# Kernel tuning notes

Hardware: AMD Instinct MI355X
Metric: run time of the kernel (lower is better)

Reference implementation:

```python
import jax, jax.numpy as jnp
import numpy as np

B = 16          # graphs per batch
N = 8192        # nodes per graph (equal-size graphs)
D = 256         # in_channels
RATIO = 0.5
K = int(np.ceil(RATIO * N))   # nodes kept per graph (PyG: ceil(ratio*N))
E = 2_097_152   # total edges (~avg_degree 16)


def setup_inputs() -> dict:
    key = jax.random.key(0)
    k1, k2, k3 = jax.random.split(key, 3)
    x = jax.random.normal(k1, (B * N, D), dtype=jnp.float32)
    # edges confined within each graph: local endpoint ids + graph offset
    local = jax.random.randint(k2, (2, E), 0, N)
    graph_of_edge = jnp.arange(E) // (E // B)            # [E]
    edge_index = local + graph_of_edge[None, :] * N      # [2, E] global node ids
    batch = jnp.repeat(jnp.arange(B), N)                 # [B*N]
    weight = jax.random.normal(k3, (D,), dtype=jnp.float32)  # TopKPooling score weight
    return {"x": x, "edge_index": edge_index, "batch": batch, "weight": weight}


def reference(x, edge_index, batch, weight):
    total = x.shape[0]
    # PyG TopKPooling: score = tanh((x . w) / ||w||)
    score = jnp.tanh((x @ weight) / jnp.linalg.norm(weight))   # [B*N]
    # per-graph top-k (equal-size graphs -> reshape)
    vals, idx = jax.lax.top_k(score.reshape(B, N), K)          # [B, K] each
    perm = (idx + jnp.arange(B)[:, None] * N).reshape(-1)      # [B*K] global kept ids
    x_out = x[perm] * vals.reshape(-1, 1)                      # gate features by score
    batch_out = batch[perm]
    # reindex: kept node i (in perm order) gets new id i, others -1 (PyG filter_adj)
    mapping = jnp.full((total,), -1, dtype=jnp.int32).at[perm].set(
        jnp.arange(B * K, dtype=jnp.int32))
    new_src = mapping[edge_index[0]]
    new_dst = mapping[edge_index[1]]
    kept = (new_src >= 0) & (new_dst >= 0)
    # fixed-shape padded edge_index: surviving edges reindexed, dropped edges = -1
    new_edge_index = jnp.where(kept[None, :], jnp.stack([new_src, new_dst]), -1)
    return x_out, new_edge_index, batch_out
```

## Files before the change

kernel.cpp:

```cpp
#include <hip/hip_runtime.h>

#define BGRAPH  16
#define NPG     8192
#define DIM     256
#define KKEEP   4096
#define TOTALN  (BGRAPH * NPG)
#define TOTKEEP (BGRAPH * KKEEP)
#define NEDGE   2097152
#define NBUCK   8192

using u16 = unsigned short;
using u32 = unsigned int;

__device__ __forceinline__ u32 desc_key(float f) {
  u32 b = __float_as_uint(f);
  u32 s = b ^ ((b & 0x80000000u) ? 0xFFFFFFFFu : 0x80000000u);
  return ~s;
}

__global__ __launch_bounds__(256) void k_score(const float* __restrict__ x,
                                               const float* __restrict__ w,
                                               float* __restrict__ score,
                                               u32* __restrict__ map32) {
  int gid  = blockIdx.x * 256 + threadIdx.x;
  if (gid < TOTALN / 2) map32[gid] = 0xFFFFFFFFu;
  int wv   = gid >> 6;
  int lane = gid & 63;
  size_t r0 = (size_t)(wv * 2);
  const float4 w4 = *reinterpret_cast<const float4*>(w + lane * 4);
  const float4 a  = *reinterpret_cast<const float4*>(x + r0 * DIM + lane * 4);
  const float4 b  = *reinterpret_cast<const float4*>(x + (r0 + 1) * DIM + lane * 4);
  float w2 = w4.x * w4.x + w4.y * w4.y + w4.z * w4.z + w4.w * w4.w;
  float d0 = a.x * w4.x + a.y * w4.y + a.z * w4.z + a.w * w4.w;
  float d1 = b.x * w4.x + b.y * w4.y + b.z * w4.z + b.w * w4.w;
  #pragma unroll
  for (int off = 32; off > 0; off >>= 1) {
    d0 += __shfl_xor(d0, off, 64);
    d1 += __shfl_xor(d1, off, 64);
    w2 += __shfl_xor(w2, off, 64);
  }
  if (lane == 0) {
    float rn = sqrtf(w2);
    score[r0]     = tanhf(d0 / rn);
    score[r0 + 1] = tanhf(d1 / rn);
  }
}

__global__ __launch_bounds__(1024) void k_sort(const float* __restrict__ score,
                                               u32* __restrict__ skey,
                                               u32* __restrict__ bends,
                                               u32* __restrict__ gceil) {
  __shared__ u32 hist[NBUCK];
  __shared__ u32 wsum[16];
  __shared__ u32 sbb;
  const int g    = blockIdx.x;
  const int tid  = threadIdx.x;
  const int wid  = tid >> 6;
  const int lane = tid & 63;
  const float* gs = score + ((size_t)g << 13);
  u32* skg = skey  + ((size_t)g << 13);
  u32* beg = bends + ((size_t)g << 13);

  #pragma unroll
  for (int i = 0; i < NBUCK / 1024; ++i) hist[tid + i * 1024] = 0;
  __syncthreads();

  u32 kd_[NPG / 1024];
  #pragma unroll
  for (int i = 0; i < NPG / 1024; ++i) {
    kd_[i] = desc_key(gs[tid + i * 1024]);
    atomicAdd(&hist[kd_[i] >> 19], 1u);
  }
  __syncthreads();

  u32 h[8], s = 0;
  #pragma unroll
  for (int j = 0; j < 8; ++j) { h[j] = hist[8 * tid + j]; s += h[j]; }
  u32 inc = s;
  #pragma unroll
  for (int off = 1; off < 64; off <<= 1) {
    u32 t = __shfl_up(inc, off, 64);
    if (lane >= off) inc += t;
  }
  if (lane == 63) wsum[wid] = inc;
  __syncthreads();
  if (tid < 16) {
    u32 v = wsum[tid], vi = v;
    #pragma unroll
    for (int off = 1; off < 16; off <<= 1) {
      u32 t = __shfl_up(vi, off, 64);
      if (tid >= off) vi += t;
    }
    wsum[tid] = vi - v;
  }
  __syncthreads();
  u32 run = inc - s + wsum[wid];
  #pragma unroll
  for (int j = 0; j < 8; ++j) {
    u32 hv  = h[j];
    u32 end = run + hv;
    hist[8 * tid + j] = run;
    beg[8 * tid + j]  = end;
    if (run < KKEEP && end >= KKEEP) {
      gceil[g] = end;
      sbb = (u32)(8 * tid + j);
    }
    run = end;
  }
  __syncthreads();

  const u32 bb = sbb;
  #pragma unroll
  for (int i = 0; i < NPG / 1024; ++i) {
    u32 kd = kd_[i];
    u32 b  = kd >> 19;
    if (b <= bb) {
      u32 pos = atomicAdd(&hist[b], 1u);
      skg[pos] = (kd << 13) | (u32)(tid + i * 1024);
    }
  }
}

__global__ __launch_bounds__(512) void k_count(const float* __restrict__ score,
                                               const u32* __restrict__ skey,
                                               const u32* __restrict__ bends,
                                               const u32* __restrict__ gceil,
                                               u16* __restrict__ map16,
                                               u16* __restrict__ inv) {
  const int g = blockIdx.x >> 4;
  const int p = (blockIdx.x & 15) * 512 + (int)threadIdx.x;
  if ((u32)p >= gceil[g]) return;
  const size_t gb = ((size_t)g << 13);
  const u32* skg = skey + gb;
  u32 key = skg[p];
  int idx = (int)(key & 0x1FFFu);
  u32 b = desc_key(score[gb + idx]) >> 19;
  const u32* beg = bends + gb;
  u32 start = b ? beg[b - 1] : 0;
  u32 end   = beg[b];
  u32 cnt = 0, q = start;
  u32 qa = (start + 3u) & ~3u;
  for (; q < qa && q < end; ++q) cnt += (skg[q] < key);
  for (; q + 4 <= end; q += 4) {
    uint4 v4 = *reinterpret_cast<const uint4*>(skg + q);
    cnt += (v4.x < key) + (v4.y < key) + (v4.z < key) + (v4.w < key);
  }
  for (; q < end; ++q) cnt += (skg[q] < key);
  u32 rank = start + cnt;
  if (rank < KKEEP) {
    map16[gb + idx] = (u16)rank;
    inv[((u32)g << 12) | rank] = (u16)idx;
  }
}

#define GB 16384
#define EB 1024

__global__ __launch_bounds__(256) void k_ge(const float* __restrict__ x,
                                            const float* __restrict__ score,
                                            const u16* __restrict__ inv,
                                            const int* __restrict__ ei,
                                            const u16* __restrict__ map16,
                                            float* __restrict__ x_out,
                                            float* __restrict__ e_out,
                                            float* __restrict__ b_out) {
  const int blk = blockIdx.x;
  const int tid = threadIdx.x;
  if (blk < GB) {
    int r    = blk * 4 + (tid >> 6);
    int lane = tid & 63;
    int idx  = (int)inv[r];
    int node = ((r >> 12) << 13) | idx;
    float val = score[node];
    const float4 v = *reinterpret_cast<const float4*>(x + (size_t)node * DIM + lane * 4);
    float4 o;
    o.x = v.x * val; o.y = v.y * val; o.z = v.z * val; o.w = v.w * val;
    *reinterpret_cast<float4*>(x_out + (size_t)r * DIM + lane * 4) = o;
    return;
  }
  int t = (blk - GB) * 256 + tid;
  size_t e8 = (size_t)t * 8;
  const int4 a0 = *reinterpret_cast<const int4*>(ei + e8);
  const int4 a1 = *reinterpret_cast<const int4*>(ei + e8 + 4);
  const int4 d0 = *reinterpret_cast<const int4*>(ei + NEDGE + e8);
  const int4 d1 = *reinterpret_cast<const int4*>(ei + NEDGE + e8 + 4);
  float4 s0, s1, dd0, dd1;
  {
    u16 ra0 = map16[a0.x], ra1 = map16[a0.y], ra2 = map16[a0.z], ra3 = map16[a0.w];
    u16 rb0 = map16[d0.x], rb1 = map16[d0.y], rb2 = map16[d0.z], rb3 = map16[d0.w];
    bool k0 = (ra0 != 0xFFFFu) && (rb0 != 0xFFFFu);
    bool k1 = (ra1 != 0xFFFFu) && (rb1 != 0xFFFFu);
    bool k2 = (ra2 != 0xFFFFu) && (rb2 != 0xFFFFu);
    bool k3 = (ra3 != 0xFFFFu) && (rb3 != 0xFFFFu);
    s0.x  = k0 ? (float)(((a0.x >> 13) << 12) | ra0) : -1.0f;
    s0.y  = k1 ? (float)(((a0.y >> 13) << 12) | ra1) : -1.0f;
    s0.z  = k2 ? (float)(((a0.z >> 13) << 12) | ra2) : -1.0f;
    s0.w  = k3 ? (float)(((a0.w >> 13) << 12) | ra3) : -1.0f;
    dd0.x = k0 ? (float)(((d0.x >> 13) << 12) | rb0) : -1.0f;
    dd0.y = k1 ? (float)(((d0.y >> 13) << 12) | rb1) : -1.0f;
    dd0.z = k2 ? (float)(((d0.z >> 13) << 12) | rb2) : -1.0f;
    dd0.w = k3 ? (float)(((d0.w >> 13) << 12) | rb3) : -1.0f;
  }
  {
    u16 ra0 = map16[a1.x], ra1 = map16[a1.y], ra2 = map16[a1.z], ra3 = map16[a1.w];
    u16 rb0 = map16[d1.x], rb1 = map16[d1.y], rb2 = map16[d1.z], rb3 = map16[d1.w];
    bool k0 = (ra0 != 0xFFFFu) && (rb0 != 0xFFFFu);
    bool k1 = (ra1 != 0xFFFFu) && (rb1 != 0xFFFFu);
    bool k2 = (ra2 != 0xFFFFu) && (rb2 != 0xFFFFu);
    bool k3 = (ra3 != 0xFFFFu) && (rb3 != 0xFFFFu);
    s1.x  = k0 ? (float)(((a1.x >> 13) << 12) | ra0) : -1.0f;
    s1.y  = k1 ? (float)(((a1.y >> 13) << 12) | ra1) : -1.0f;
    s1.z  = k2 ? (float)(((a1.z >> 13) << 12) | ra2) : -1.0f;
    s1.w  = k3 ? (float)(((a1.w >> 13) << 12) | ra3) : -1.0f;
    dd1.x = k0 ? (float)(((d1.x >> 13) << 12) | rb0) : -1.0f;
    dd1.y = k1 ? (float)(((d1.y >> 13) << 12) | rb1) : -1.0f;
    dd1.z = k2 ? (float)(((d1.z >> 13) << 12) | rb2) : -1.0f;
    dd1.w = k3 ? (float)(((d1.w >> 13) << 12) | rb3) : -1.0f;
  }
  *reinterpret_cast<float4*>(e_out + e8)             = s0;
  *reinterpret_cast<float4*>(e_out + e8 + 4)         = s1;
  *reinterpret_cast<float4*>(e_out + NEDGE + e8)     = dd0;
  *reinterpret_cast<float4*>(e_out + NEDGE + e8 + 4) = dd1;
  if (t < TOTKEEP / 4) {
    float gf = (float)(t >> 10);
    float4 bo; bo.x = gf; bo.y = gf; bo.z = gf; bo.w = gf;
    *reinterpret_cast<float4*>(b_out + 4 * (size_t)t) = bo;
  }
}

extern "C" void kernel_launch(void* const* d_in, const int* in_sizes, int n_in,
                              void* d_out, int out_size, void* d_ws, size_t ws_size,
                              hipStream_t stream) {
  const float* x  = nullptr;
  const int*   ei = nullptr;
  const float* w  = nullptr;
  for (int i = 0; i < n_in; ++i) {
    if      (in_sizes[i] == TOTALN * DIM) x  = (const float*)d_in[i];
    else if (in_sizes[i] == 2 * NEDGE)    ei = (const int*)d_in[i];
    else if (in_sizes[i] == DIM)          w  = (const float*)d_in[i];
  }
  (void)out_size; (void)ws_size;

  float* out   = (float*)d_out;
  float* x_out = out;
  float* e_out = out + (size_t)TOTKEEP * DIM;
  float* b_out = e_out + 2 * (size_t)NEDGE;

  char* ws = (char*)d_ws;
  float* score = (float*)(ws);
  u32*   skey  = (u32*)(ws + (512  << 10));
  u32*   bends = (u32*)(ws + (1024 << 10));
  u16*   map16 = (u16*)(ws + (1536 << 10));
  u16*   inv   = (u16*)(ws + (1792 << 10));
  u32*   gceil = (u32*)(ws + (1920 << 10));

  hipLaunchKernelGGL(k_score, dim3(TOTALN / 8),  dim3(256),  0, stream,
                     x, w, score, (u32*)map16);
  hipLaunchKernelGGL(k_sort,  dim3(BGRAPH),      dim3(1024), 0, stream,
                     score, skey, bends, gceil);
  hipLaunchKernelGGL(k_count, dim3(BGRAPH * 16), dim3(512),  0, stream,
                     score, skey, bends, gceil, map16, inv);
  hipLaunchKernelGGL(k_ge,    dim3(GB + EB),     dim3(256),  0, stream,
                     x, score, inv, ei, map16, x_out, e_out, b_out);
}
```

Measured before the change: 77.08 us.

## Fuse rank counting into sort kernel and score four rows per wave

```diff
diff --git a/kernel.cpp b/kernel.cpp
--- a/kernel.cpp
+++ b/kernel.cpp
@@ -26,30 +26,38 @@
   if (gid < TOTALN / 2) map32[gid] = 0xFFFFFFFFu;
   int wv   = gid >> 6;
   int lane = gid & 63;
-  size_t r0 = (size_t)(wv * 2);
+  size_t r0 = (size_t)wv * 4;
   const float4 w4 = *reinterpret_cast<const float4*>(w + lane * 4);
-  const float4 a  = *reinterpret_cast<const float4*>(x + r0 * DIM + lane * 4);
+  const float4 a  = *reinterpret_cast<const float4*>(x + (r0    ) * DIM + lane * 4);
   const float4 b  = *reinterpret_cast<const float4*>(x + (r0 + 1) * DIM + lane * 4);
+  const float4 c  = *reinterpret_cast<const float4*>(x + (r0 + 2) * DIM + lane * 4);
+  const float4 d  = *reinterpret_cast<const float4*>(x + (r0 + 3) * DIM + lane * 4);
   float w2 = w4.x * w4.x + w4.y * w4.y + w4.z * w4.z + w4.w * w4.w;
   float d0 = a.x * w4.x + a.y * w4.y + a.z * w4.z + a.w * w4.w;
   float d1 = b.x * w4.x + b.y * w4.y + b.z * w4.z + b.w * w4.w;
+  float d2 = c.x * w4.x + c.y * w4.y + c.z * w4.z + c.w * w4.w;
+  float d3 = d.x * w4.x + d.y * w4.y + d.z * w4.z + d.w * w4.w;
   #pragma unroll
   for (int off = 32; off > 0; off >>= 1) {
     d0 += __shfl_xor(d0, off, 64);
     d1 += __shfl_xor(d1, off, 64);
+    d2 += __shfl_xor(d2, off, 64);
+    d3 += __shfl_xor(d3, off, 64);
     w2 += __shfl_xor(w2, off, 64);
   }
   if (lane == 0) {
     float rn = sqrtf(w2);
     score[r0]     = tanhf(d0 / rn);
     score[r0 + 1] = tanhf(d1 / rn);
+    score[r0 + 2] = tanhf(d2 / rn);
+    score[r0 + 3] = tanhf(d3 / rn);
   }
 }
 
 __global__ __launch_bounds__(1024) void k_sort(const float* __restrict__ score,
                                                u32* __restrict__ skey,
-                                               u32* __restrict__ bends,
-                                               u32* __restrict__ gceil) {
+                                               u16* __restrict__ map16,
+                                               u16* __restrict__ inv) {
   __shared__ u32 hist[NBUCK];
   __shared__ u32 wsum[16];
   __shared__ u32 sbb;
@@ -58,8 +66,7 @@
   const int wid  = tid >> 6;
   const int lane = tid & 63;
   const float* gs = score + ((size_t)g << 13);
-  u32* skg = skey  + ((size_t)g << 13);
-  u32* beg = bends + ((size_t)g << 13);
+  u32* skg = skey + ((size_t)g << 13);
 
   #pragma unroll
   for (int i = 0; i < NBUCK / 1024; ++i) hist[tid + i * 1024] = 0;
@@ -100,16 +107,13 @@
     u32 hv  = h[j];
     u32 end = run + hv;
     hist[8 * tid + j] = run;
-    beg[8 * tid + j]  = end;
-    if (run < KKEEP && end >= KKEEP) {
-      gceil[g] = end;
-      sbb = (u32)(8 * tid + j);
-    }
+    if (run < KKEEP && end >= KKEEP) sbb = (u32)(8 * tid + j);
     run = end;
   }
   __syncthreads();
 
   const u32 bb = sbb;
+  u32 pos_[NPG / 1024];
   #pragma unroll
   for (int i = 0; i < NPG / 1024; ++i) {
     u32 kd = kd_[i];
@@ -117,39 +121,35 @@
     if (b <= bb) {
       u32 pos = atomicAdd(&hist[b], 1u);
       skg[pos] = (kd << 13) | (u32)(tid + i * 1024);
-    }
-  }
-}
-
-__global__ __launch_bounds__(512) void k_count(const float* __restrict__ score,
-                                               const u32* __restrict__ skey,
-                                               const u32* __restrict__ bends,
-                                               const u32* __restrict__ gceil,
-                                               u16* __restrict__ map16,
-                                               u16* __restrict__ inv) {
-  const int g = blockIdx.x >> 4;
-  const int p = (blockIdx.x & 15) * 512 + (int)threadIdx.x;
-  if ((u32)p >= gceil[g]) return;
-  const size_t gb = ((size_t)g << 13);
-  const u32* skg = skey + gb;
-  u32 key = skg[p];
-  int idx = (int)(key & 0x1FFFu);
-  u32 b = desc_key(score[gb + idx]) >> 19;
-  const u32* beg = bends + gb;
-  u32 start = b ? beg[b - 1] : 0;
-  u32 end   = beg[b];
-  u32 cnt = 0, q = start;
-  u32 qa = (start + 3u) & ~3u;
-  for (; q < qa && q < end; ++q) cnt += (skg[q] < key);
-  for (; q + 4 <= end; q += 4) {
-    uint4 v4 = *reinterpret_cast<const uint4*>(skg + q);
-    cnt += (v4.x < key) + (v4.y < key) + (v4.z < key) + (v4.w < key);
-  }
-  for (; q < end; ++q) cnt += (skg[q] < key);
-  u32 rank = start + cnt;
-  if (rank < KKEEP) {
-    map16[gb + idx] = (u16)rank;
-    inv[((u32)g << 12) | rank] = (u16)idx;
+      pos_[i] = pos;
+    } else {
+      pos_[i] = 0xFFFFFFFFu;
+    }
+  }
+  __syncthreads();
+
+  #pragma unroll
+  for (int i = 0; i < NPG / 1024; ++i) {
+    if (pos_[i] == 0xFFFFFFFFu) continue;
+    u32 kd  = kd_[i];
+    u32 b   = kd >> 19;
+    int idx = tid + i * 1024;
+    u32 key = (kd << 13) | (u32)idx;
+    u32 start = b ? hist[b - 1] : 0;
+    u32 end   = hist[b];
+    u32 cnt = 0, q = start;
+    u32 qa = (start + 3u) & ~3u;
+    for (; q < qa && q < end; ++q) cnt += (skg[q] < key);
+    for (; q + 4 <= end; q += 4) {
+      uint4 v4 = *reinterpret_cast<const uint4*>(skg + q);
+      cnt += (v4.x < key) + (v4.y < key) + (v4.z < key) + (v4.w < key);
+    }
+    for (; q < end; ++q) cnt += (skg[q] < key);
+    u32 rank = start + cnt;
+    if (rank < KKEEP) {
+      map16[((size_t)g << 13) + idx] = (u16)rank;
+      inv[((u32)g << 12) | rank] = (u16)idx;
+    }
   }
 }
 
@@ -249,17 +249,13 @@
   char* ws = (char*)d_ws;
   float* score = (float*)(ws);
   u32*   skey  = (u32*)(ws + (512  << 10));
-  u32*   bends = (u32*)(ws + (1024 << 10));
-  u16*   map16 = (u16*)(ws + (1536 << 10));
-  u16*   inv   = (u16*)(ws + (1792 << 10));
-  u32*   gceil = (u32*)(ws + (1920 << 10));
-
-  hipLaunchKernelGGL(k_score, dim3(TOTALN / 8),  dim3(256),  0, stream,
+  u16*   map16 = (u16*)(ws + (1024 << 10));
+  u16*   inv   = (u16*)(ws + (1280 << 10));
+
+  hipLaunchKernelGGL(k_score, dim3(TOTALN / 16), dim3(256),  0, stream,
                      x, w, score, (u32*)map16);
   hipLaunchKernelGGL(k_sort,  dim3(BGRAPH),      dim3(1024), 0, stream,
-                     score, skey, bends, gceil);
-  hipLaunchKernelGGL(k_count, dim3(BGRAPH * 16), dim3(512),  0, stream,
-                     score, skey, bends, gceil, map16, inv);
+                     score, skey, map16, inv);
   hipLaunchKernelGGL(k_ge,    dim3(GB + EB),     dim3(256),  0, stream,
                      x, score, inv, ei, map16, x_out, e_out, b_out);
 }
```

After: 139.4 us. +80.8%, slower.
